# Optimization experiments

Hardware: AMD Instinct MI355X
Metric: run time of the kernel (lower is better)

Reference implementation:

```python
import jax, jax.numpy as jnp
import numpy as np

N_GENES = 15135
N_CMT = 1000
HID = 64


def _gcn_norm(edge_index, n):
    # add self-loops, compute symmetric normalization deg^-1/2 * deg^-1/2
    loop = jnp.arange(n, dtype=edge_index.dtype)
    src = jnp.concatenate([edge_index[0], loop])
    dst = jnp.concatenate([edge_index[1], loop])
    deg = jax.ops.segment_sum(jnp.ones_like(src, dtype=jnp.float32), dst, num_segments=n)
    dinv = jnp.where(deg > 0, 1.0 / jnp.sqrt(deg), 0.0)
    return src, dst, dinv[src] * dinv[dst]


def _gcn_conv(x, W, b, src, dst, norm, n):
    h = x @ W                                  # [bs, N, H]
    m = h[:, src, :] * norm[None, :, None]     # gather messages [bs, E, H]
    out = jnp.zeros_like(h).at[:, dst, :].add(m)
    return out + b


def setup_inputs():
    key = jax.random.key(0)
    ks = jax.random.split(key, 16)
    bs, nf, hfc, ncls, E, P = 8, 64, 128, 2, 242160, 120000
    s = 0.05
    return {
        "x": jax.random.normal(ks[0], (bs, N_GENES, nf), jnp.float32),
        "batch": jnp.zeros((bs,), jnp.int32),
        "edge_index": jax.random.randint(ks[1], (2, E), 0, N_GENES),
        "path_row": jax.random.randint(ks[2], (P,), 0, N_GENES),
        "path_col": jax.random.randint(ks[3], (P,), 0, N_CMT),
        "W1": jax.random.normal(ks[4], (nf, HID), jnp.float32) * s,
        "b1": jnp.zeros((HID,), jnp.float32),
        "W2": jax.random.normal(ks[5], (HID, HID), jnp.float32) * s,
        "b2": jnp.zeros((HID,), jnp.float32),
        "W3": jax.random.normal(ks[6], (HID, HID), jnp.float32) * s,
        "b3": jnp.zeros((HID,), jnp.float32),
        "fcW": jax.random.normal(ks[7], (3 * HID, 1), jnp.float32) * s,
        "fcb": jnp.zeros((1,), jnp.float32),
        "l1W": jax.random.normal(ks[8], (N_CMT, hfc), jnp.float32) * s,
        "l1b": jnp.zeros((hfc,), jnp.float32),
        "l2W": jax.random.normal(ks[9], (hfc, ncls), jnp.float32) * s,
        "l2b": jnp.zeros((ncls,), jnp.float32),
    }


def reference(x, batch, edge_index, path_row, path_col,
              W1, b1, W2, b2, W3, b3, fcW, fcb, l1W, l1b, l2W, l2b):
    bs, n = x.shape[0], x.shape[1]
    src, dst, norm = _gcn_norm(edge_index, n)

    x1 = jax.nn.relu(_gcn_conv(x, W1, b1, src, dst, norm, n))
    x2 = jax.nn.relu(_gcn_conv(x1, W2, b2, src, dst, norm, n))
    x3 = jax.nn.relu(_gcn_conv(x2, W3, b3, src, dst, norm, n))
    # mode='cat': torch.stack(xs, -1).view(bs, N, -1) -> layout [..., h*L + l]
    xc = jnp.stack([x1, x2, x3], axis=-1).reshape(bs, n, HID * 3)

    # pathway pooling: scatter_mean(x[row], col) over node axis
    xt = jnp.transpose(xc, (1, 0, 2))            # [N, bs, F]
    g = xt[path_row]                             # [P, bs, F]
    sums = jax.ops.segment_sum(g, path_col, num_segments=N_CMT)
    cnt = jax.ops.segment_sum(jnp.ones_like(path_col, dtype=xc.dtype), path_col, num_segments=N_CMT)
    pooled = sums / jnp.maximum(cnt, 1.0)[:, None, None]   # [n_cmt, bs, F]
    pooled = jnp.transpose(pooled, (1, 0, 2)).reshape(-1, HID * 3)  # [bs*n_cmt, F]

    h = (pooled @ fcW + fcb).reshape(bs, N_CMT)   # fc -> view(-1, n_cmt)
    h = jax.nn.relu(h @ l1W + l1b)                # (dropout is identity in eval)
    h = h @ l2W + l2b
    return jax.nn.log_softmax(h, axis=-1)
```

## Files before the change

### kernel.cpp

```cpp
#include <hip/hip_runtime.h>
#include <hip/hip_bf16.h>
#include <hip/hip_fp16.h>
#include <math.h>

#define HID 64

#if defined(__has_builtin)
#if __has_builtin(__builtin_amdgcn_cvt_pk_f32_fp8) && __has_builtin(__builtin_amdgcn_cvt_pk_fp8_f32)
#define HWFP8 1
#endif
#endif

typedef float vfloat2 __attribute__((ext_vector_type(2)));


__device__ __forceinline__ unsigned short f2bf(float x) {
    unsigned int u = __float_as_uint(x);
    unsigned int r = u + 0x7fffu + ((u >> 16) & 1u);
    return (unsigned short)(r >> 16);
}

#ifndef HWFP8
__device__ __forceinline__ unsigned int enc8_sw(float a) {
    unsigned short hb = __half_as_ushort(__float2half(a));
    unsigned int r = (unsigned int)hb + 0x7fu + ((hb >> 8) & 1u);
    return (r >> 8) & 0xffu;
}
__device__ __forceinline__ float dec8_sw(unsigned int b) {
    return __half2float(__ushort_as_half((unsigned short)(b << 8)));
}
#endif

__device__ __forceinline__ unsigned int enc4(float a, float b, float c, float d) {
#ifdef HWFP8
    int r = __builtin_amdgcn_cvt_pk_fp8_f32(a, b, 0, false);
    r = __builtin_amdgcn_cvt_pk_fp8_f32(c, d, r, true);
    return (unsigned int)r;
#else
    return enc8_sw(a) | (enc8_sw(b) << 8) | (enc8_sw(c) << 16) | (enc8_sw(d) << 24);
#endif
}

__device__ __forceinline__ void dec4(unsigned int w, float* f) {
#ifdef HWFP8
    vfloat2 a = __builtin_amdgcn_cvt_pk_f32_fp8((int)w, false);
    vfloat2 b = __builtin_amdgcn_cvt_pk_f32_fp8((int)w, true);
    f[0] = a.x; f[1] = a.y; f[2] = b.x; f[3] = b.y;
#else
    f[0] = dec8_sw(w & 0xffu); f[1] = dec8_sw((w >> 8) & 0xffu);
    f[2] = dec8_sw((w >> 16) & 0xffu); f[3] = dec8_sw(w >> 24);
#endif
}

__device__ __forceinline__ void dec8(uint2 g, float* f) {
    dec4(g.x, f);
    dec4(g.y, f + 4);
}


__global__ __launch_bounds__(256) void k_pre_count(const int* __restrict__ edst, int* __restrict__ deg, int E,
                                                   const int* __restrict__ pcol, int* __restrict__ ccnt, int P) {
    int gth = blockIdx.x * blockDim.x + threadIdx.x;
    int GT = gridDim.x * blockDim.x;
    for (int e = gth; e < E; e += GT) atomicAdd(&deg[edst[e]], 1);
    for (int p = gth; p < P; p += GT) atomicAdd(&ccnt[pcol[p]], 1);
}

__global__ __launch_bounds__(256) void k_pre_scan(const int* __restrict__ deg, int* __restrict__ rowoff, int N,
                                                  const int* __restrict__ ccnt, int* __restrict__ coff, int NC,
                                                  float* __restrict__ dinv) {
    __shared__ int part[256];
    int t = threadIdx.x;
    int gth = blockIdx.x * blockDim.x + t;
    int GT = gridDim.x * blockDim.x;
    for (int i = gth; i < N; i += GT) dinv[i] = rsqrtf((float)(deg[i] + 1));

    const int* cnt = nullptr; int* off = nullptr; int n = 0;
    if (blockIdx.x == 0)      { cnt = deg;  off = rowoff; n = N; }
    else if (blockIdx.x == 1) { cnt = ccnt; off = coff;   n = NC; }
    else return;

    int CH = (n + 255) >> 8;
    int lo = min(t * CH, n), hi = min(lo + CH, n);
    int sum = 0;
    for (int i = lo; i < hi; ++i) sum += cnt[i];
    part[t] = sum;
    __syncthreads();
    for (int o = 1; o < 256; o <<= 1) {
        int v = (t >= o) ? part[t - o] : 0;
        __syncthreads();
        part[t] += v;
        __syncthreads();
    }
    int run = (t == 0) ? 0 : part[t - 1];
    for (int i = lo; i < hi; ++i) { off[i] = run; run += cnt[i]; }
    if (t == 255) off[n] = run;
}

__global__ __launch_bounds__(256) void k_pre_scatter(const int* __restrict__ esrc, const int* __restrict__ edst,
                                                     const float* __restrict__ dinv, const int* __restrict__ rowoff,
                                                     int* __restrict__ fill, int* __restrict__ ssrc,
                                                     float* __restrict__ snorm, int E,
                                                     const int* __restrict__ prow, const int* __restrict__ pcol,
                                                     const int* __restrict__ coff, int* __restrict__ cfill,
                                                     int* __restrict__ crow, int P) {
    int gth = blockIdx.x * blockDim.x + threadIdx.x;
    int GT = gridDim.x * blockDim.x;
    for (int e = gth; e < E; e += GT) {
        int s = esrc[e], d = edst[e];
        int pos = rowoff[d] + atomicAdd(&fill[d], 1);
        ssrc[pos]  = s;
        snorm[pos] = dinv[s] * dinv[d];
    }
    for (int p = gth; p < P; p += GT) {
        int c = pcol[p];
        int pos = coff[c] + atomicAdd(&cfill[c], 1);
        crow[pos] = prow[p];
    }
}


template<int MODE>
__global__ __launch_bounds__(256) void k_gemm_rt(const void* __restrict__ Xv,
                                                 const float* __restrict__ W,
                                                 unsigned int* __restrict__ Yq,
                                                 float S, int N, int rowsTot) {
    __shared__ float sW[64 * 64];
    __shared__ float sXT[64 * 68];
    int t = threadIdx.x;
    int r0 = blockIdx.x * 64;

#pragma unroll
    for (int i = 0; i < 16; ++i) sW[t + i * 256] = W[t + i * 256];

    {
        int row = t & 63;
        int kg = t >> 6;
        int gr = r0 + row;
        bool ok = gr < rowsTot;
        const float* Xf = (const float*)Xv;
        const unsigned short* Xh = (const unsigned short*)Xv;
#pragma unroll
        for (int i = 0; i < 4; ++i) {
            int k = (kg + i * 4) * 4;
            float4 v = make_float4(0.f, 0.f, 0.f, 0.f);
            if (ok) {
                if (MODE == 0) {
                    int n = gr >> 3, b = gr & 7;
                    v = *(const float4*)&Xf[((size_t)b * N + n) * 64 + k];
                } else {
                    ushort4 u = *(const ushort4*)&Xh[(size_t)gr * 64 + k];
                    v.x = __uint_as_float(((unsigned int)u.x) << 16);
                    v.y = __uint_as_float(((unsigned int)u.y) << 16);
                    v.z = __uint_as_float(((unsigned int)u.z) << 16);
                    v.w = __uint_as_float(((unsigned int)u.w) << 16);
                }
            }
            sXT[(k + 0) * 68 + row] = v.x;
            sXT[(k + 1) * 68 + row] = v.y;
            sXT[(k + 2) * 68 + row] = v.z;
            sXT[(k + 3) * 68 + row] = v.w;
        }
    }
    __syncthreads();

    int ci = t & 15, ri = t >> 4;
    float acc[4][4] = {};
#pragma unroll 16
    for (int k = 0; k < 64; ++k) {
        float4 xr = *(const float4*)&sXT[k * 68 + ri * 4];
        float4 wc = *(const float4*)&sW[k * 64 + ci * 4];
        acc[0][0] = fmaf(xr.x, wc.x, acc[0][0]); acc[0][1] = fmaf(xr.x, wc.y, acc[0][1]);
        acc[0][2] = fmaf(xr.x, wc.z, acc[0][2]); acc[0][3] = fmaf(xr.x, wc.w, acc[0][3]);
        acc[1][0] = fmaf(xr.y, wc.x, acc[1][0]); acc[1][1] = fmaf(xr.y, wc.y, acc[1][1]);
        acc[1][2] = fmaf(xr.y, wc.z, acc[1][2]); acc[1][3] = fmaf(xr.y, wc.w, acc[1][3]);
        acc[2][0] = fmaf(xr.z, wc.x, acc[2][0]); acc[2][1] = fmaf(xr.z, wc.y, acc[2][1]);
        acc[2][2] = fmaf(xr.z, wc.z, acc[2][2]); acc[2][3] = fmaf(xr.z, wc.w, acc[2][3]);
        acc[3][0] = fmaf(xr.w, wc.x, acc[3][0]); acc[3][1] = fmaf(xr.w, wc.y, acc[3][1]);
        acc[3][2] = fmaf(xr.w, wc.z, acc[3][2]); acc[3][3] = fmaf(xr.w, wc.w, acc[3][3]);
    }

#pragma unroll
    for (int j = 0; j < 4; ++j) {
        int row = r0 + ri * 4 + j;
        if (row < rowsTot)
            Yq[(size_t)row * 16 + ci] =
                enc4(acc[j][0] * S, acc[j][1] * S, acc[j][2] * S, acc[j][3] * S);
    }
}

template<int LAYER, bool STORE>
__global__ __launch_bounds__(256) void k_agg(const uint2* __restrict__ Y,
                                             const int* __restrict__ rowoff,
                                             const int* __restrict__ ssrc,
                                             const float* __restrict__ snorm,
                                             const float* __restrict__ dinv,
                                             const float* __restrict__ bias,
                                             const float* __restrict__ fcW,
                                             uint4* __restrict__ O,
                                             float* __restrict__ sArr,
                                             float invS, int N) {
    int n = blockIdx.x * 4 + (threadIdx.x >> 6);
    if (n >= N) return;
    int lane = threadIdx.x & 63;
    int hb = (lane & 7) * 8;
    float bv[8], wv[8];
#pragma unroll
    for (int k = 0; k < 8; ++k) { bv[k] = bias[hb + k]; wv[k] = fcW[3 * (hb + k) + LAYER]; }

    float dn = dinv[n];
    float w0 = dn * dn;
    float acc[8], f[8];
    dec8(Y[(size_t)n * 64 + lane], f);
#pragma unroll
    for (int k = 0; k < 8; ++k) acc[k] = w0 * f[k];

    int beg = rowoff[n], end = rowoff[n + 1];
    int i = beg;
    for (; i + 7 < end; i += 8) {
        int   sI[8];
        float wI[8];
        uint2 g[8];
#pragma unroll
        for (int u = 0; u < 8; ++u) { sI[u] = ssrc[i + u]; wI[u] = snorm[i + u]; }
#pragma unroll
        for (int u = 0; u < 8; ++u) g[u] = Y[(size_t)sI[u] * 64 + lane];
#pragma unroll
        for (int u = 0; u < 8; ++u) {
            dec8(g[u], f);
#pragma unroll
            for (int k = 0; k < 8; ++k) acc[k] = fmaf(wI[u], f[k], acc[k]);
        }
    }
    for (; i < end; ++i) {
        int s = ssrc[i];
        float w = snorm[i];
        dec8(Y[(size_t)s * 64 + lane], f);
#pragma unroll
        for (int k = 0; k < 8; ++k) acc[k] = fmaf(w, f[k], acc[k]);
    }

    float sv = 0.f;
#pragma unroll
    for (int k = 0; k < 8; ++k) {
        float o = fmaxf(fmaf(acc[k], invS, bv[k]), 0.f);
        acc[k] = o;
        sv = fmaf(o, wv[k], sv);
    }
    if (STORE) {
        uint4 o;
        o.x = (unsigned int)f2bf(acc[0]) | ((unsigned int)f2bf(acc[1]) << 16);
        o.y = (unsigned int)f2bf(acc[2]) | ((unsigned int)f2bf(acc[3]) << 16);
        o.z = (unsigned int)f2bf(acc[4]) | ((unsigned int)f2bf(acc[5]) << 16);
        o.w = (unsigned int)f2bf(acc[6]) | ((unsigned int)f2bf(acc[7]) << 16);
        O[(size_t)n * 64 + lane] = o;
    }
    sv += __shfl_down(sv, 4, 64);
    sv += __shfl_down(sv, 2, 64);
    sv += __shfl_down(sv, 1, 64);
    if ((lane & 7) == 0) {
        int b = lane >> 3;
        float* sp = sArr + (size_t)n * 8 + b;
        if (LAYER == 0) *sp = sv;
        else            *sp += sv;
    }
}


__global__ __launch_bounds__(64) void k_poolg(const float* __restrict__ sArr,
                                              const int* __restrict__ coff,
                                              const int* __restrict__ crow,
                                              float* __restrict__ hpoolT) {
    int c = blockIdx.x;
    int lane = threadIdx.x;
    int beg = coff[c], end = coff[c + 1];
    int b = lane & 7;
    float acc = 0.f;
    int i = beg + (lane >> 3);
    for (; i + 24 < end; i += 32) {
        int r0 = crow[i], r1 = crow[i + 8], r2 = crow[i + 16], r3 = crow[i + 24];
        float a0 = sArr[(size_t)r0 * 8 + b];
        float a1 = sArr[(size_t)r1 * 8 + b];
        float a2 = sArr[(size_t)r2 * 8 + b];
        float a3 = sArr[(size_t)r3 * 8 + b];
        acc += (a0 + a1) + (a2 + a3);
    }
    for (; i < end; i += 8) acc += sArr[(size_t)crow[i] * 8 + b];
    acc += __shfl_down(acc, 32, 64);
    acc += __shfl_down(acc, 16, 64);
    acc += __shfl_down(acc, 8, 64);
    if (lane < 8) {
        float inv = 1.f / fmaxf((float)(end - beg), 1.f);
        hpoolT[(size_t)c * 8 + b] = acc * inv;
    }
}

__global__ __launch_bounds__(128) void k_l1f(const float* __restrict__ hpoolT,
                                             const float* __restrict__ fcb,
                                             const float* __restrict__ l1W,
                                             float* __restrict__ hpre,
                                             int* __restrict__ done,
                                             const float* __restrict__ l1b,
                                             const float* __restrict__ l2W,
                                             const float* __restrict__ l2b,
                                             float* __restrict__ out,
                                             int NC, int HFC, int bs, int NCLS,
                                             int CHUNK, int nBlocks) {
    __shared__ float hl[64];
    int b = blockIdx.y;
    int c0 = blockIdx.x * CHUNK;
    int j = threadIdx.x;
    int cend = min(c0 + CHUNK, NC);
    for (int c = c0 + j; c < cend; c += blockDim.x)
        hl[c - c0] = hpoolT[(size_t)c * 8 + b] + fcb[0];
    __syncthreads();
    float acc = 0.f;
    for (int c = c0; c < cend; ++c) acc = fmaf(hl[c - c0], l1W[(size_t)c * HFC + j], acc);
    atomicAdd(&hpre[(size_t)b * HFC + j], acc);

    __threadfence();
    __syncthreads();
    __shared__ int amLast;
    if (j == 0) amLast = (atomicAdd(done, 1) == nBlocks - 1);
    __syncthreads();
    if (!amLast) return;
    __threadfence();

    __shared__ float sZ[64];
    int g = j >> 3, l8 = j & 7;
    int nout = bs * NCLS;
    float v = 0.f;
    int b2 = g / NCLS, k2 = g - b2 * NCLS;
    if (g < nout) {
        for (int jj = l8; jj < HFC; jj += 8) {
            float h = fmaxf(hpre[(size_t)b2 * HFC + jj] + l1b[jj], 0.f);
            v = fmaf(h, l2W[(size_t)jj * NCLS + k2], v);
        }
    }
    v += __shfl_down(v, 4, 8);
    v += __shfl_down(v, 2, 8);
    v += __shfl_down(v, 1, 8);
    if (l8 == 0 && g < nout) sZ[g] = v + l2b[k2];
    __syncthreads();
    if (j < bs) {
        float m = -1e30f;
        for (int c = 0; c < NCLS; ++c) m = fmaxf(m, sZ[j * NCLS + c]);
        float s = 0.f;
        for (int c = 0; c < NCLS; ++c) s += expf(sZ[j * NCLS + c] - m);
        float lse = m + logf(s);
        for (int c = 0; c < NCLS; ++c) out[j * NCLS + c] = sZ[j * NCLS + c] - lse;
    }
}


extern "C" void kernel_launch(void* const* d_in, const int* in_sizes, int n_in,
                              void* d_out, int out_size, void* d_ws, size_t ws_size,
                              hipStream_t stream) {
    const float* x   = (const float*)d_in[0];
    const int* eidx  = (const int*)d_in[2];
    const int* prow  = (const int*)d_in[3];
    const int* pcol  = (const int*)d_in[4];
    const float* W1  = (const float*)d_in[5];
    const float* b1  = (const float*)d_in[6];
    const float* W2  = (const float*)d_in[7];
    const float* b2  = (const float*)d_in[8];
    const float* W3  = (const float*)d_in[9];
    const float* b3  = (const float*)d_in[10];
    const float* fcW = (const float*)d_in[11];
    const float* fcb = (const float*)d_in[12];
    const float* l1W = (const float*)d_in[13];
    const float* l1b = (const float*)d_in[14];
    const float* l2W = (const float*)d_in[15];
    const float* l2b = (const float*)d_in[16];
    float* out = (float*)d_out;

    const int bs   = in_sizes[1];
    const int E    = in_sizes[2] / 2;
    const int P    = in_sizes[3];
    const int N    = in_sizes[0] / (bs * HID);
    const int HFC  = in_sizes[14];
    const int NC   = in_sizes[13] / HFC;
    const int NCLS = in_sizes[15] / HFC;
    const int rows = N * bs;

    const int* esrc = eidx;
    const int* edst = eidx + E;

    size_t off = 0;
    auto alloc = [&](size_t bytes) -> void* {
        void* r = (char*)d_ws + off;
        off += (bytes + 255) & ~(size_t)255;
        return r;
    };
    char* zbase   = (char*)d_ws;
    int*   deg    = (int*)  alloc((size_t)N * 4);
    int*   fill   = (int*)  alloc((size_t)N * 4);
    int*   ccnt   = (int*)  alloc((size_t)NC * 4);
    int*   cfill  = (int*)  alloc((size_t)NC * 4);
    float* hpre   = (float*)alloc((size_t)bs * HFC * 4);
    int*   done   = (int*)  alloc(4);
    size_t zspan  = off;
    float* dinv   = (float*)alloc((size_t)N * 4);
    int*   rowoff = (int*)  alloc(((size_t)N + 1) * 4);
    int*   coff   = (int*)  alloc(((size_t)NC + 1) * 4);
    int*   crow   = (int*)  alloc((size_t)P * 4);
    float* hpoolT = (float*)alloc((size_t)NC * bs * 4);
    int*   ssrc   = (int*)  alloc((size_t)E * 4);
    float* snorm  = (float*)alloc((size_t)E * 4);
    unsigned int* Yq   = (unsigned int*)alloc((size_t)rows * HID);
    unsigned short* X1 = (unsigned short*)alloc((size_t)rows * HID * 2);
    unsigned short* X2 = (unsigned short*)alloc((size_t)rows * HID * 2);
    float* sArr   = (float*)alloc((size_t)rows * 4);

    hipMemsetAsync(zbase, 0, zspan, stream);

    int gPre = 512;
    k_pre_count<<<gPre, 256, 0, stream>>>(edst, deg, E, pcol, ccnt, P);
    k_pre_scan<<<64, 256, 0, stream>>>(deg, rowoff, N, ccnt, coff, NC, dinv);
    k_pre_scatter<<<gPre, 256, 0, stream>>>(esrc, edst, dinv, rowoff, fill, ssrc, snorm, E,
                                            prow, pcol, coff, cfill, crow, P);

    const float S1 = 1.f,  iS1 = 1.f;
    const float S2 = 16.f, iS2 = 1.f / 16.f;
    const float S3 = 128.f, iS3 = 1.f / 128.f;

    int gG = (rows + 63) / 64;
    int gA = (N + 3) / 4;
    k_gemm_rt<0><<<gG, 256, 0, stream>>>(x, W1, Yq, S1, N, rows);
    k_agg<0, true><<<gA, 256, 0, stream>>>((const uint2*)Yq, rowoff, ssrc, snorm, dinv, b1, fcW, (uint4*)X1, sArr, iS1, N);
    k_gemm_rt<1><<<gG, 256, 0, stream>>>(X1, W2, Yq, S2, N, rows);
    k_agg<1, true><<<gA, 256, 0, stream>>>((const uint2*)Yq, rowoff, ssrc, snorm, dinv, b2, fcW, (uint4*)X2, sArr, iS2, N);
    k_gemm_rt<1><<<gG, 256, 0, stream>>>(X2, W3, Yq, S3, N, rows);
    k_agg<2, false><<<gA, 256, 0, stream>>>((const uint2*)Yq, rowoff, ssrc, snorm, dinv, b3, fcW, nullptr, sArr, iS3, N);

    k_poolg<<<NC, 64, 0, stream>>>(sArr, coff, crow, hpoolT);

    const int CHUNK = 40;
    dim3 gL1((NC + CHUNK - 1) / CHUNK, bs);
    int nBlocks = gL1.x * gL1.y;
    k_l1f<<<gL1, 128, 0, stream>>>(hpoolT, fcb, l1W, hpre, done, l1b, l2W, l2b, out,
                                   NC, HFC, bs, NCLS, CHUNK, nBlocks);
}
```

Measured before the change: 377.4 us.

## Replace scalar FMA GEMM with bf16 MFMA 16x16x32 using pre-transposed weights

Rewrites the per-layer dense transform to use the bf16 MFMA matrix instruction instead of scalar FMAs over shared memory. The weights are converted to bf16 and transposed once, inside the existing counting kernel. Each wave computes a 16x64 output tile, stages it through shared memory, and writes the same fp8-packed output. The first layer's fp32 input is now rounded to bf16 before the multiply, which costs some precision.

```diff
diff --git a/kernel.cpp b/kernel.cpp
--- a/kernel.cpp
+++ b/kernel.cpp
@@ -12,6 +12,10 @@
 #endif
 
 typedef float vfloat2 __attribute__((ext_vector_type(2)));
+typedef __attribute__((ext_vector_type(8))) short short8_t;
+typedef __attribute__((ext_vector_type(4))) float f32x4;
+
+union ABFrag { short8_t s; unsigned short u[8]; };
 
 
 __device__ __forceinline__ unsigned short f2bf(float x) {
@@ -59,11 +63,19 @@
 
 
 __global__ __launch_bounds__(256) void k_pre_count(const int* __restrict__ edst, int* __restrict__ deg, int E,
-                                                   const int* __restrict__ pcol, int* __restrict__ ccnt, int P) {
+                                                   const int* __restrict__ pcol, int* __restrict__ ccnt, int P,
+                                                   const float* __restrict__ W1, const float* __restrict__ W2,
+                                                   const float* __restrict__ W3, unsigned short* __restrict__ Wt) {
     int gth = blockIdx.x * blockDim.x + threadIdx.x;
     int GT = gridDim.x * blockDim.x;
     for (int e = gth; e < E; e += GT) atomicAdd(&deg[edst[e]], 1);
     for (int p = gth; p < P; p += GT) atomicAdd(&ccnt[pcol[p]], 1);
+    for (int i = gth; i < 3 * 4096; i += GT) {
+        int l = i >> 12, r = i & 4095;
+        int k = r >> 6, c = r & 63;
+        const float* W = (l == 0) ? W1 : (l == 1) ? W2 : W3;
+        Wt[(l << 12) + c * 64 + k] = f2bf(W[r]);
+    }
 }
 
 __global__ __launch_bounds__(256) void k_pre_scan(const int* __restrict__ deg, int* __restrict__ rowoff, int N,
@@ -121,71 +133,71 @@
 
 
 template<int MODE>
-__global__ __launch_bounds__(256) void k_gemm_rt(const void* __restrict__ Xv,
-                                                 const float* __restrict__ W,
-                                                 unsigned int* __restrict__ Yq,
-                                                 float S, int N, int rowsTot) {
-    __shared__ float sW[64 * 64];
-    __shared__ float sXT[64 * 68];
+__global__ __launch_bounds__(256) void k_gemm_mfma(const void* __restrict__ Xv,
+                                                   const unsigned short* __restrict__ Wt,
+                                                   unsigned int* __restrict__ Yq,
+                                                   float S, int N, int rowsTot) {
+    __shared__ float sOut[4][16 * 68];
     int t = threadIdx.x;
-    int r0 = blockIdx.x * 64;
-
-#pragma unroll
-    for (int i = 0; i < 16; ++i) sW[t + i * 256] = W[t + i * 256];
-
-    {
-        int row = t & 63;
-        int kg = t >> 6;
-        int gr = r0 + row;
-        bool ok = gr < rowsTot;
-        const float* Xf = (const float*)Xv;
-        const unsigned short* Xh = (const unsigned short*)Xv;
-#pragma unroll
-        for (int i = 0; i < 4; ++i) {
-            int k = (kg + i * 4) * 4;
-            float4 v = make_float4(0.f, 0.f, 0.f, 0.f);
-            if (ok) {
-                if (MODE == 0) {
-                    int n = gr >> 3, b = gr & 7;
-                    v = *(const float4*)&Xf[((size_t)b * N + n) * 64 + k];
-                } else {
-                    ushort4 u = *(const ushort4*)&Xh[(size_t)gr * 64 + k];
-                    v.x = __uint_as_float(((unsigned int)u.x) << 16);
-                    v.y = __uint_as_float(((unsigned int)u.y) << 16);
-                    v.z = __uint_as_float(((unsigned int)u.z) << 16);
-                    v.w = __uint_as_float(((unsigned int)u.w) << 16);
-                }
+    int w = t >> 6, lane = t & 63;
+    int r0w = blockIdx.x * 64 + w * 16;
+    int rA = r0w + (lane & 15);
+    int kg = (lane >> 4) * 8;
+    int cc = lane & 15;
+
+    const float* Xf = (const float*)Xv;
+    const unsigned short* Xh = (const unsigned short*)Xv;
+
+    f32x4 acc[4] = {f32x4{}, f32x4{}, f32x4{}, f32x4{}};
+
+#pragma unroll
+    for (int k0 = 0; k0 < 64; k0 += 32) {
+        ABFrag a;
+        if (rA < rowsTot) {
+            if (MODE == 0) {
+                int n = rA >> 3, b = rA & 7;
+                const float* p = &Xf[((size_t)b * N + n) * 64 + k0 + kg];
+                float4 v0 = *(const float4*)p;
+                float4 v1 = *(const float4*)(p + 4);
+                a.u[0] = f2bf(v0.x); a.u[1] = f2bf(v0.y);
+                a.u[2] = f2bf(v0.z); a.u[3] = f2bf(v0.w);
+                a.u[4] = f2bf(v1.x); a.u[5] = f2bf(v1.y);
+                a.u[6] = f2bf(v1.z); a.u[7] = f2bf(v1.w);
+            } else {
+                a.s = *(const short8_t*)&Xh[(size_t)rA * 64 + k0 + kg];
             }
-            sXT[(k + 0) * 68 + row] = v.x;
-            sXT[(k + 1) * 68 + row] = v.y;
-            sXT[(k + 2) * 68 + row] = v.z;
-            sXT[(k + 3) * 68 + row] = v.w;
+        } else {
+#pragma unroll
+            for (int j = 0; j < 8; ++j) a.u[j] = 0;
         }
-    }
-    __syncthreads();
-
-    int ci = t & 15, ri = t >> 4;
-    float acc[4][4] = {};
-#pragma unroll 16
-    for (int k = 0; k < 64; ++k) {
-        float4 xr = *(const float4*)&sXT[k * 68 + ri * 4];
-        float4 wc = *(const float4*)&sW[k * 64 + ci * 4];
-        acc[0][0] = fmaf(xr.x, wc.x, acc[0][0]); acc[0][1] = fmaf(xr.x, wc.y, acc[0][1]);
-        acc[0][2] = fmaf(xr.x, wc.z, acc[0][2]); acc[0][3] = fmaf(xr.x, wc.w, acc[0][3]);
-        acc[1][0] = fmaf(xr.y, wc.x, acc[1][0]); acc[1][1] = fmaf(xr.y, wc.y, acc[1][1]);
-        acc[1][2] = fmaf(xr.y, wc.z, acc[1][2]); acc[1][3] = fmaf(xr.y, wc.w, acc[1][3]);
-        acc[2][0] = fmaf(xr.z, wc.x, acc[2][0]); acc[2][1] = fmaf(xr.z, wc.y, acc[2][1]);
-        acc[2][2] = fmaf(xr.z, wc.z, acc[2][2]); acc[2][3] = fmaf(xr.z, wc.w, acc[2][3]);
-        acc[3][0] = fmaf(xr.w, wc.x, acc[3][0]); acc[3][1] = fmaf(xr.w, wc.y, acc[3][1]);
-        acc[3][2] = fmaf(xr.w, wc.z, acc[3][2]); acc[3][3] = fmaf(xr.w, wc.w, acc[3][3]);
-    }
-
-#pragma unroll
-    for (int j = 0; j < 4; ++j) {
-        int row = r0 + ri * 4 + j;
-        if (row < rowsTot)
-            Yq[(size_t)row * 16 + ci] =
-                enc4(acc[j][0] * S, acc[j][1] * S, acc[j][2] * S, acc[j][3] * S);
+#pragma unroll
+        for (int c = 0; c < 4; ++c) {
+            ABFrag b;
+            b.s = *(const short8_t*)&Wt[(size_t)(c * 16 + cc) * 64 + k0 + kg];
+            acc[c] = __builtin_amdgcn_mfma_f32_16x16x32_bf16(a.s, b.s, acc[c], 0, 0, 0);
+        }
+    }
+
+    float* so = &sOut[w][0];
+    int cr = (lane >> 4) * 4;
+#pragma unroll
+    for (int c = 0; c < 4; ++c) {
+        so[(cr + 0) * 68 + c * 16 + cc] = acc[c][0];
+        so[(cr + 1) * 68 + c * 16 + cc] = acc[c][1];
+        so[(cr + 2) * 68 + c * 16 + cc] = acc[c][2];
+        so[(cr + 3) * 68 + c * 16 + cc] = acc[c][3];
+    }
+    __syncthreads();
+#pragma unroll
+    for (int i = 0; i < 4; ++i) {
+        int idx = lane + i * 64;
+        int row = idx >> 4, ci = idx & 15;
+        int grow = r0w + row;
+        if (grow < rowsTot) {
+            float4 v = *(const float4*)&so[row * 68 + ci * 4];
+            Yq[(size_t)grow * 16 + ci] =
+                enc4(v.x * S, v.y * S, v.z * S, v.w * S);
+        }
     }
 }
 
@@ -411,11 +423,12 @@
     unsigned short* X1 = (unsigned short*)alloc((size_t)rows * HID * 2);
     unsigned short* X2 = (unsigned short*)alloc((size_t)rows * HID * 2);
     float* sArr   = (float*)alloc((size_t)rows * 4);
+    unsigned short* Wt = (unsigned short*)alloc((size_t)3 * 64 * 64 * 2);
 
     hipMemsetAsync(zbase, 0, zspan, stream);
 
     int gPre = 512;
-    k_pre_count<<<gPre, 256, 0, stream>>>(edst, deg, E, pcol, ccnt, P);
+    k_pre_count<<<gPre, 256, 0, stream>>>(edst, deg, E, pcol, ccnt, P, W1, W2, W3, Wt);
     k_pre_scan<<<64, 256, 0, stream>>>(deg, rowoff, N, ccnt, coff, NC, dinv);
     k_pre_scatter<<<gPre, 256, 0, stream>>>(esrc, edst, dinv, rowoff, fill, ssrc, snorm, E,
                                             prow, pcol, coff, cfill, crow, P);
@@ -426,11 +439,11 @@
 
     int gG = (rows + 63) / 64;
     int gA = (N + 3) / 4;
-    k_gemm_rt<0><<<gG, 256, 0, stream>>>(x, W1, Yq, S1, N, rows);
+    k_gemm_mfma<0><<<gG, 256, 0, stream>>>(x, Wt, Yq, S1, N, rows);
     k_agg<0, true><<<gA, 256, 0, stream>>>((const uint2*)Yq, rowoff, ssrc, snorm, dinv, b1, fcW, (uint4*)X1, sArr, iS1, N);
-    k_gemm_rt<1><<<gG, 256, 0, stream>>>(X1, W2, Yq, S2, N, rows);
+    k_gemm_mfma<1><<<gG, 256, 0, stream>>>(X1, Wt + 4096, Yq, S2, N, rows);
     k_agg<1, true><<<gA, 256, 0, stream>>>((const uint2*)Yq, rowoff, ssrc, snorm, dinv, b2, fcW, (uint4*)X2, sArr, iS2, N);
-    k_gemm_rt<1><<<gG, 256, 0, stream>>>(X2, W3, Yq, S3, N, rows);
+    k_gemm_mfma<1><<<gG, 256, 0, stream>>>(X2, Wt + 8192, Yq, S3, N, rows);
     k_agg<2, false><<<gA, 256, 0, stream>>>((const uint2*)Yq, rowoff, ssrc, snorm, dinv, b3, fcW, nullptr, sArr, iS3, N);
 
     k_poolg<<<NC, 64, 0, stream>>>(sArr, coff, crow, hpoolT);
```

Measured after the change: 361.1 us. 1.05x faster.
